# Performance work log

Hardware: AMD Instinct MI355X
Metric: run time of the kernel (lower is better)

Reference implementation:

```python
import jax, jax.numpy as jnp
import numpy as np

E = 1_600_000      # num edges
N = 50_000         # num nodes
G = 100            # num graphs in batch
EMB = 128          # emb_size
OUT = 256          # out_emb_size
NRAD = 6           # num_radial
NDENSE = 3         # num_dense


def setup_inputs() -> dict:
    key = jax.random.key(0)
    ks = jax.random.split(key, 8)
    m = jax.random.normal(ks[0], (E, EMB), dtype=jnp.float32)
    rbf = jax.random.normal(ks[1], (E, NRAD), dtype=jnp.float32)
    src = jax.random.randint(ks[2], (E,), 0, N, dtype=jnp.int64)
    graph_ids = jnp.sort(jax.random.randint(ks[3], (N,), 0, G, dtype=jnp.int64))
    # parameters (torch Linear convention: W [out, in])
    W_rbf = jax.random.normal(ks[4], (EMB, NRAD), dtype=jnp.float32) / np.sqrt(NRAD)
    W_up = jax.random.normal(ks[5], (OUT, EMB), dtype=jnp.float32) / np.sqrt(EMB)
    W_dense = jax.random.normal(ks[6], (NDENSE, OUT, OUT), dtype=jnp.float32) / np.sqrt(OUT)
    b_dense = jnp.zeros((NDENSE, OUT), dtype=jnp.float32)
    return {"m": m, "rbf": rbf, "src": src, "graph_ids": graph_ids,
            "W_rbf": W_rbf, "W_up": W_up, "W_dense": W_dense, "b_dense": b_dense}


def reference(m, rbf, src, graph_ids, W_rbf, W_up, W_dense, b_dense):
    # edge transform: tmp = m * dense_rbf(rbf)            [E, EMB]
    tmp = m * jnp.einsum('er,fr->ef', rbf, W_rbf)
    # reverse-graph copy_e/sum == scatter-sum onto original src nodes
    t = jax.ops.segment_sum(tmp, src, num_segments=N)     # [N, EMB]
    # up projection (no bias)
    t = jnp.einsum('ne,oe->no', t, W_up)                  # [N, OUT]
    # dense MLP with SiLU
    for i in range(NDENSE):
        t = jax.nn.silu(jnp.einsum('no,po->np', t, W_dense[i]) + b_dense[i])
    # extensive readout: per-graph sum
    out = jax.ops.segment_sum(t, graph_ids, num_segments=G)  # [G, OUT]
    return out
```

## Files before the change

### kernel.cpp

```cpp
#include <hip/hip_runtime.h>
#include <hip/hip_bf16.h>

typedef __attribute__((ext_vector_type(8))) short short8;
typedef __attribute__((ext_vector_type(4))) float f32x4;

#define EMB 128
#define OUT 256
#define NRAD 6
#define NDENSE 3
#define BSH 7
#define MAXBKT 512
#define HB 128

static __device__ __forceinline__ unsigned short f32_to_bf16(float f) {
    union { float f; unsigned u; } v; v.f = f;
    unsigned r = v.u + 0x7fffu + ((v.u >> 16) & 1u);
    return (unsigned short)(r >> 16);
}
static __device__ __forceinline__ float silu(float x) {
    return x / (1.f + __expf(-x));
}
static __device__ __forceinline__ void gload_lds16(const void* gp, void* lp) {
    __builtin_amdgcn_global_load_lds(
        (const __attribute__((address_space(1))) void*)gp,
        (__attribute__((address_space(3))) void*)lp, 16, 0, 0);
}

__global__ __launch_bounds__(256) void setup_hist_kernel(
        const int* __restrict__ src, int* __restrict__ bpart,
        const float* __restrict__ Wup, const float* __restrict__ Wd,
        unsigned short* __restrict__ Wbf, float* __restrict__ out,
        int E, int nbkt, int outn) {
    __shared__ int h[MAXBKT];
    for (int b = threadIdx.x; b < nbkt; b += 256) h[b] = 0;
    __syncthreads();
    int gtid = blockIdx.x * blockDim.x + threadIdx.x;
    int stride = gridDim.x * blockDim.x;
    for (int e = gtid; e < E; e += stride)
        atomicAdd(&h[src[e] >> BSH], 1);
    for (int j = gtid; j < outn; j += stride) out[j] = 0.f;
    const int n1 = OUT * EMB, n2 = NDENSE * OUT * OUT;
    for (int j = gtid; j < n1 + n2; j += stride)
        Wbf[j] = f32_to_bf16(j < n1 ? Wup[j] : Wd[j - n1]);
    __syncthreads();
    int* row = bpart + (size_t)blockIdx.x * MAXBKT;
    for (int b = threadIdx.x; b < nbkt; b += 256) row[b] = h[b];
}

__global__ __launch_bounds__(512) void bscan_kernel(
        const int* __restrict__ bpart, int* __restrict__ bbase,
        int* __restrict__ gcursor, int nbkt, int E) {
    __shared__ int s[MAXBKT];
    int t = threadIdx.x;
    int v = 0;
    if (t < nbkt) {
#pragma unroll 8
        for (int k = 0; k < HB; ++k) v += bpart[(size_t)k * MAXBKT + t];
    }
    s[t] = v;
    __syncthreads();
    for (int d = 1; d < MAXBKT; d <<= 1) {
        int x = (t >= d) ? s[t - d] : 0;
        __syncthreads();
        s[t] += x;
        __syncthreads();
    }
    if (t < nbkt) {
        int ex = s[t] - v;
        bbase[t] = ex;
        gcursor[t] = ex;
    }
    if (t == 0) bbase[nbkt] = E;
}

__global__ __launch_bounds__(256) void bscatter_kernel(
        const int* __restrict__ src, int* __restrict__ gcursor,
        int* __restrict__ pairs, int E, int nbkt) {
    __shared__ int h[MAXBKT];
    __shared__ int base[MAXBKT];
    for (int b = threadIdx.x; b < nbkt; b += 256) h[b] = 0;
    __syncthreads();
    const int per = (E + gridDim.x - 1) / gridDim.x;
    const int e0 = blockIdx.x * per;
    const int e1 = min(e0 + per, E);
    for (int e = e0 + threadIdx.x; e < e1; e += 256)
        atomicAdd(&h[src[e] >> BSH], 1);
    __syncthreads();
    for (int b = threadIdx.x; b < nbkt; b += 256)
        base[b] = h[b] ? atomicAdd(&gcursor[b], h[b]) : 0;
    __syncthreads();
    for (int e = e0 + threadIdx.x; e < e1; e += 256) {
        int s = src[e];
        int pos = atomicAdd(&base[s >> BSH], 1);
        pairs[pos] = (e << BSH) | (s & ((1 << BSH) - 1));
    }
}

__global__ __launch_bounds__(256) void local_csr_kernel(
        const int* __restrict__ pairs, const int* __restrict__ bbase,
        int* __restrict__ offsets, int* __restrict__ perm, int N, int E, int nbkt) {
    __shared__ int cnt[128], exc[128], cur[128];
    const int b = blockIdx.x;
    const int t = threadIdx.x;
    const int n0 = b << BSH;
    const int nn = min(128, N - n0);
    const int p0 = bbase[b], p1 = bbase[b + 1];
    if (t < 128) cnt[t] = 0;
    __syncthreads();
    for (int i = p0 + t; i < p1; i += 256)
        atomicAdd(&cnt[pairs[i] & 127], 1);
    __syncthreads();
    if (t < 128) exc[t] = cnt[t];
    __syncthreads();
    for (int d = 1; d < 128; d <<= 1) {
        int x = (t >= d && t < 128) ? exc[t - d] : 0;
        __syncthreads();
        if (t < 128) exc[t] += x;
        __syncthreads();
    }
    if (t < 128) {
        int ex = exc[t] - cnt[t];
        cur[t] = ex;
        if (t < nn) offsets[n0 + t] = p0 + ex;
    }
    if (b == 0 && t == 0) offsets[N] = E;
    __syncthreads();
    for (int i = p0 + t; i < p1; i += 256) {
        int pr = pairs[i];
        int pos = p0 + atomicAdd(&cur[pr & 127], 1);
        perm[pos] = pr >> BSH;
    }
}

__global__ __launch_bounds__(256) void edge_accum_kernel(
        const float* __restrict__ m, const float* __restrict__ rbf,
        const int* __restrict__ perm, const int* __restrict__ offsets,
        const float* __restrict__ W_rbf, uint2* __restrict__ t_pack, int N) {
    const int lane = threadIdx.x & 63;
    const int h = lane >> 5;
    const int c = lane & 31;
    const int gw = blockIdx.x * (blockDim.x >> 6) + (threadIdx.x >> 6);
    const int nwaves = gridDim.x * (blockDim.x >> 6);

    float wk[4][6];
#pragma unroll
    for (int k = 0; k < 4; ++k)
#pragma unroll
        for (int j = 0; j < 6; ++j) wk[k][j] = W_rbf[(4 * c + k) * NRAD + j];

    for (int node = gw; node < N; node += nwaves) {
        const int beg = offsets[node], end = offsets[node + 1];
        float a0 = 0.f, a1 = 0.f, a2 = 0.f, a3 = 0.f;
        int pe = 0;
        if (beg < end) {
            int pi = beg + (lane & 31); if (pi > end - 1) pi = end - 1;
            pe = perm[pi];
        }
        for (int cb = beg; cb < end; cb += 32) {
            int pe_next = 0;
            if (cb + 32 < end) {
                int pi = cb + 32 + (lane & 31); if (pi > end - 1) pi = end - 1;
                pe_next = perm[pi];
            }
            const int rem = end - cb;
            const int np = (rem >= 32) ? 16 : ((rem + 1) >> 1);
#pragma unroll 4
            for (int p = 0; p < np; ++p) {
                int e = __shfl(pe, 2 * p + h);
                const float2* rp = (const float2*)(rbf + (size_t)e * NRAD);
                float2 r0 = rp[0], r1 = rp[1], r2 = rp[2];
                float4 mv = *(const float4*)(m + (size_t)e * EMB + 4 * c);
                float g = (2 * p + h < rem) ? 1.f : 0.f;
                float p0 = (wk[0][0]*r0.x + wk[0][1]*r0.y + wk[0][2]*r1.x
                          + wk[0][3]*r1.y + wk[0][4]*r2.x + wk[0][5]*r2.y) * g;
                float p1 = (wk[1][0]*r0.x + wk[1][1]*r0.y + wk[1][2]*r1.x
                          + wk[1][3]*r1.y + wk[1][4]*r2.x + wk[1][5]*r2.y) * g;
                float p2 = (wk[2][0]*r0.x + wk[2][1]*r0.y + wk[2][2]*r1.x
                          + wk[2][3]*r1.y + wk[2][4]*r2.x + wk[2][5]*r2.y) * g;
                float p3 = (wk[3][0]*r0.x + wk[3][1]*r0.y + wk[3][2]*r1.x
                          + wk[3][3]*r1.y + wk[3][4]*r2.x + wk[3][5]*r2.y) * g;
                a0 = fmaf(mv.x, p0, a0);
                a1 = fmaf(mv.y, p1, a1);
                a2 = fmaf(mv.z, p2, a2);
                a3 = fmaf(mv.w, p3, a3);
            }
            pe = pe_next;
        }
        a0 += __shfl_xor(a0, 32);
        a1 += __shfl_xor(a1, 32);
        a2 += __shfl_xor(a2, 32);
        a3 += __shfl_xor(a3, 32);
        if (h == 0) {
            uint2 pk;
            pk.x = (unsigned)f32_to_bf16(a0) | ((unsigned)f32_to_bf16(a1) << 16);
            pk.y = (unsigned)f32_to_bf16(a2) | ((unsigned)f32_to_bf16(a3) << 16);
            t_pack[(size_t)node * 32 + c] = pk;
        }
    }
}

__global__ __launch_bounds__(512) void fused_mlp2_kernel(
        const unsigned short* __restrict__ A0,
        const unsigned short* __restrict__ Wup,
        const unsigned short* __restrict__ Wd,
        const float* __restrict__ bd,
        const int* __restrict__ gids,
        float* __restrict__ out, int M) {
    __shared__ char Abuf[65536];
    __shared__ char Wbuf[32768];
    const int t    = threadIdx.x;
    const int w    = t >> 6;
    const int lane = t & 63;
    const int r    = lane & 15;
    const int g    = lane >> 4;
    const int wrh  = (w >> 2) * 64;
    const int wc   = w & 3;
    const int row0 = blockIdx.x * 128;

    f32x4 acc[4][4];

#pragma unroll
    for (int it = 0; it < 4; ++it) {
        int unit = it * 512 + t;
        int row  = unit >> 4;
        int seg  = unit & 15;
        int csrc = (seg * 16) ^ ((row & 7) << 4);
        int ga = row0 + row; if (ga >= M) ga = M - 1;
        gload_lds16((const char*)A0 + (size_t)ga * 256 + csrc, Abuf + unit * 16);
    }

#pragma unroll
    for (int i = 0; i < 4; ++i)
#pragma unroll
        for (int j = 0; j < 4; ++j) acc[i][j] = (f32x4){0.f, 0.f, 0.f, 0.f};
#pragma unroll
    for (int kci = 0; kci < 2; ++kci) {
        const int kc = kci * 64;
        if (kci) __syncthreads();
#pragma unroll
        for (int it = 0; it < 4; ++it) {
            int unit = it * 512 + t;
            int wrow = unit >> 3;
            int seg  = unit & 7;
            int csrc = (seg * 16) ^ ((wrow & 7) << 4);
            gload_lds16((const char*)Wup + (size_t)wrow * 256 + kc * 2 + csrc,
                        Wbuf + unit * 16);
        }
        asm volatile("s_waitcnt vmcnt(0)" ::: "memory");
        __syncthreads();
#pragma unroll
        for (int ks = 0; ks < 2; ++ks) {
            short8 af[4], bf[4];
#pragma unroll
            for (int mi = 0; mi < 4; ++mi) {
                int row = wrh + mi * 16 + r;
                int off = kc * 2 + ks * 64 + g * 16;
                af[mi] = *(const short8*)(Abuf + row * 256 + (off ^ ((row & 7) << 4)));
            }
#pragma unroll
            for (int nj = 0; nj < 4; ++nj) {
                int col = wc * 64 + nj * 16 + r;
                bf[nj] = *(const short8*)(Wbuf + col * 128
                          + ((ks * 64 + g * 16) ^ ((col & 7) << 4)));
            }
#pragma unroll
            for (int mi = 0; mi < 4; ++mi)
#pragma unroll
                for (int nj = 0; nj < 4; ++nj)
                    acc[mi][nj] = __builtin_amdgcn_mfma_f32_16x16x32_bf16(
                        af[mi], bf[nj], acc[mi][nj], 0, 0, 0);
        }
    }
    __syncthreads();
#pragma unroll
    for (int mi = 0; mi < 4; ++mi)
#pragma unroll
        for (int nj = 0; nj < 4; ++nj)
#pragma unroll
            for (int q = 0; q < 4; ++q) {
                int row = wrh + mi * 16 + g * 4 + q;
                int col = wc * 64 + nj * 16 + r;
                *(unsigned short*)(Abuf + row * 512 + ((col * 2) ^ ((row & 7) << 4)))
                    = f32_to_bf16(acc[mi][nj][q]);
            }
    __syncthreads();

    for (int ell = 0; ell < NDENSE; ++ell) {
        const unsigned short* Wl = Wd + (size_t)ell * OUT * OUT;
        const float* bias = bd + ell * OUT;
#pragma unroll
        for (int i = 0; i < 4; ++i)
#pragma unroll
            for (int j = 0; j < 4; ++j) acc[i][j] = (f32x4){0.f, 0.f, 0.f, 0.f};
#pragma unroll
        for (int kci = 0; kci < 4; ++kci) {
            const int kc = kci * 64;
            __syncthreads();
#pragma unroll
            for (int it = 0; it < 4; ++it) {
                int unit = it * 512 + t;
                int wrow = unit >> 3;
                int seg  = unit & 7;
                int csrc = (seg * 16) ^ ((wrow & 7) << 4);
                gload_lds16((const char*)Wl + (size_t)wrow * 512 + kc * 2 + csrc,
                            Wbuf + unit * 16);
            }
            asm volatile("s_waitcnt vmcnt(0)" ::: "memory");
            __syncthreads();
#pragma unroll
            for (int ks = 0; ks < 2; ++ks) {
                short8 af[4], bf[4];
#pragma unroll
                for (int mi = 0; mi < 4; ++mi) {
                    int row = wrh + mi * 16 + r;
                    int off = kc * 2 + ks * 64 + g * 16;
                    af[mi] = *(const short8*)(Abuf + row * 512 + (off ^ ((row & 7) << 4)));
                }
#pragma unroll
                for (int nj = 0; nj < 4; ++nj) {
                    int col = wc * 64 + nj * 16 + r;
                    bf[nj] = *(const short8*)(Wbuf + col * 128
                              + ((ks * 64 + g * 16) ^ ((col & 7) << 4)));
                }
#pragma unroll
                for (int mi = 0; mi < 4; ++mi)
#pragma unroll
                    for (int nj = 0; nj < 4; ++nj)
                        acc[mi][nj] = __builtin_amdgcn_mfma_f32_16x16x32_bf16(
                            af[mi], bf[nj], acc[mi][nj], 0, 0, 0);
            }
        }
        __syncthreads();
        if (ell < NDENSE - 1) {
#pragma unroll
            for (int mi = 0; mi < 4; ++mi)
#pragma unroll
                for (int nj = 0; nj < 4; ++nj) {
                    int col = wc * 64 + nj * 16 + r;
                    float b = bias[col];
#pragma unroll
                    for (int q = 0; q < 4; ++q) {
                        int row = wrh + mi * 16 + g * 4 + q;
                        *(unsigned short*)(Abuf + row * 512
                            + ((col * 2) ^ ((row & 7) << 4)))
                            = f32_to_bf16(silu(acc[mi][nj][q] + b));
                    }
                }
            __syncthreads();
        } else {
            bool uni = (row0 + 127 < M) && (gids[row0] == gids[row0 + 127]);
            if (uni) {
                int gph = gids[row0];
                float* og = out + (size_t)gph * OUT;
#pragma unroll
                for (int nj = 0; nj < 4; ++nj) {
                    int gcol = wc * 64 + nj * 16 + r;
                    float b = bias[gcol];
                    float s = 0.f;
#pragma unroll
                    for (int mi = 0; mi < 4; ++mi)
#pragma unroll
                        for (int q = 0; q < 4; ++q)
                            s += silu(acc[mi][nj][q] + b);
                    s += __shfl_xor(s, 16);
                    s += __shfl_xor(s, 32);
                    if (g == 0) atomicAdd(&og[gcol], s);
                }
            } else {
#pragma unroll
                for (int nj = 0; nj < 4; ++nj) {
                    int gcol = wc * 64 + nj * 16 + r;
                    float b = bias[gcol];
#pragma unroll
                    for (int mi = 0; mi < 4; ++mi)
#pragma unroll
                        for (int q = 0; q < 4; ++q) {
                            int grow = row0 + wrh + mi * 16 + g * 4 + q;
                            if (grow < M)
                                atomicAdd(&out[(size_t)gids[grow] * OUT + gcol],
                                          silu(acc[mi][nj][q] + b));
                        }
                }
            }
        }
    }
}

extern "C" void kernel_launch(void* const* d_in, const int* in_sizes, int n_in,
                              void* d_out, int out_size, void* d_ws, size_t ws_size,
                              hipStream_t stream) {
    const float* m         = (const float*)d_in[0];
    const float* rbf       = (const float*)d_in[1];
    const int*   src       = (const int*)d_in[2];
    const int*   gids      = (const int*)d_in[3];
    const float* W_rbf     = (const float*)d_in[4];
    const float* W_up      = (const float*)d_in[5];
    const float* W_dense   = (const float*)d_in[6];
    const float* b_dense   = (const float*)d_in[7];
    float* out = (float*)d_out;

    const int E = in_sizes[2];
    const int N = in_sizes[3];
    const int nbkt = (N + 127) >> BSH;

    size_t off = 0;
    auto alloc = [&](size_t bytes) -> void* {
        void* p = (char*)d_ws + off;
        off += (bytes + 255) & ~(size_t)255;
        return p;
    };
    int* bpart   = (int*)alloc((size_t)HB * MAXBKT * 4);
    int* bbase   = (int*)alloc((size_t)(MAXBKT + 1) * 4);
    int* gcursor = (int*)alloc((size_t)MAXBKT * 4);
    int* offsets = (int*)alloc(((size_t)N + 1) * 4);
    int* pairs   = (int*)alloc((size_t)E * 4);
    int* perm    = (int*)alloc((size_t)E * 4);
    unsigned short* t_bf = (unsigned short*)alloc((size_t)N * EMB * 2);
    unsigned short* Wbf  = (unsigned short*)alloc((size_t)(OUT * EMB + NDENSE * OUT * OUT) * 2);
    unsigned short* Wup_bf = Wbf;
    unsigned short* Wd_bf  = Wbf + OUT * EMB;

    setup_hist_kernel<<<HB, 256, 0, stream>>>(src, bpart, W_up, W_dense, Wbf,
                                              out, E, nbkt, out_size);
    bscan_kernel<<<1, MAXBKT, 0, stream>>>(bpart, bbase, gcursor, nbkt, E);
    bscatter_kernel<<<512, 256, 0, stream>>>(src, gcursor, pairs, E, nbkt);
    local_csr_kernel<<<nbkt, 256, 0, stream>>>(pairs, bbase, offsets, perm, N, E, nbkt);

    edge_accum_kernel<<<2048, 256, 0, stream>>>(m, rbf, perm, offsets, W_rbf,
                                                (uint2*)t_bf, N);

    fused_mlp2_kernel<<<(N + 127) / 128, 512, 0, stream>>>(t_bf, Wup_bf, Wd_bf,
                                                           b_dense, gids, out, N);
}
```

Baseline: 397.7 us.

## Reuse per-block histograms in scatter and double-buffer MLP weight staging

The bucket scatter no longer recomputes a per-block histogram and global cursor atomics. The scan turns each histogram block's counts into exclusive per-block offsets, and the scatter uses the same grid-stride partition to place edges directly; the histogram grid also grows to more blocks. The fused MLP kernel double-buffers weight tiles in LDS, prefetching the next k-chunk (and the next layer's first chunk) while MFMAs run on the current one. This drops a barrier per chunk at the cost of doubling the weight LDS buffer, which may reduce occupancy.

```diff
diff --git a/kernel.cpp b/kernel.cpp
--- a/kernel.cpp
+++ b/kernel.cpp
@@ -10,7 +10,7 @@
 #define NDENSE 3
 #define BSH 7
 #define MAXBKT 512
-#define HB 128
+#define HB 256
 
 static __device__ __forceinline__ unsigned short f32_to_bf16(float f) {
     union { float f; unsigned u; } v; v.f = f;
@@ -24,6 +24,17 @@
     __builtin_amdgcn_global_load_lds(
         (const __attribute__((address_space(1))) void*)gp,
         (__attribute__((address_space(3))) void*)lp, 16, 0, 0);
+}
+static __device__ __forceinline__ void stage_w(const char* Wsrc, int rowBytes,
+                                               int kcByte, char* dst, int t) {
+#pragma unroll
+    for (int it = 0; it < 4; ++it) {
+        int unit = it * 512 + t;
+        int wrow = unit >> 3;
+        int seg  = unit & 7;
+        int csrc = (seg * 16) ^ ((wrow & 7) << 4);
+        gload_lds16(Wsrc + (size_t)wrow * rowBytes + kcByte + csrc, dst + unit * 16);
+    }
 }
 
 __global__ __launch_bounds__(256) void setup_hist_kernel(
@@ -48,14 +59,16 @@
 }
 
 __global__ __launch_bounds__(512) void bscan_kernel(
-        const int* __restrict__ bpart, int* __restrict__ bbase,
-        int* __restrict__ gcursor, int nbkt, int E) {
+        int* __restrict__ bpart, int* __restrict__ bbase, int nbkt, int E) {
     __shared__ int s[MAXBKT];
     int t = threadIdx.x;
     int v = 0;
     if (t < nbkt) {
-#pragma unroll 8
-        for (int k = 0; k < HB; ++k) v += bpart[(size_t)k * MAXBKT + t];
+        for (int k = 0; k < HB; ++k) {
+            int x = bpart[(size_t)k * MAXBKT + t];
+            bpart[(size_t)k * MAXBKT + t] = v;
+            v += x;
+        }
     }
     s[t] = v;
     __syncthreads();
@@ -65,31 +78,21 @@
         s[t] += x;
         __syncthreads();
     }
-    if (t < nbkt) {
-        int ex = s[t] - v;
-        bbase[t] = ex;
-        gcursor[t] = ex;
-    }
+    if (t < nbkt) bbase[t] = s[t] - v;
     if (t == 0) bbase[nbkt] = E;
 }
 
 __global__ __launch_bounds__(256) void bscatter_kernel(
-        const int* __restrict__ src, int* __restrict__ gcursor,
-        int* __restrict__ pairs, int E, int nbkt) {
-    __shared__ int h[MAXBKT];
+        const int* __restrict__ src, const int* __restrict__ bpart,
+        const int* __restrict__ bbase, int* __restrict__ pairs, int E, int nbkt) {
     __shared__ int base[MAXBKT];
-    for (int b = threadIdx.x; b < nbkt; b += 256) h[b] = 0;
-    __syncthreads();
-    const int per = (E + gridDim.x - 1) / gridDim.x;
-    const int e0 = blockIdx.x * per;
-    const int e1 = min(e0 + per, E);
-    for (int e = e0 + threadIdx.x; e < e1; e += 256)
-        atomicAdd(&h[src[e] >> BSH], 1);
-    __syncthreads();
-    for (int b = threadIdx.x; b < nbkt; b += 256)
-        base[b] = h[b] ? atomicAdd(&gcursor[b], h[b]) : 0;
-    __syncthreads();
-    for (int e = e0 + threadIdx.x; e < e1; e += 256) {
+    const int b = blockIdx.x;
+    const int* myrow = bpart + (size_t)b * MAXBKT;
+    for (int bb = threadIdx.x; bb < nbkt; bb += 256)
+        base[bb] = myrow[bb] + bbase[bb];
+    __syncthreads();
+    int gtid = b * 256 + threadIdx.x, gs = HB * 256;
+    for (int e = gtid; e < E; e += gs) {
         int s = src[e];
         int pos = atomicAdd(&base[s >> BSH], 1);
         pairs[pos] = (e << BSH) | (s & ((1 << BSH) - 1));
@@ -207,7 +210,7 @@
         const int* __restrict__ gids,
         float* __restrict__ out, int M) {
     __shared__ char Abuf[65536];
-    __shared__ char Wbuf[32768];
+    __shared__ char Wbuf[2][32768];
     const int t    = threadIdx.x;
     const int w    = t >> 6;
     const int lane = t & 63;
@@ -229,6 +232,9 @@
         gload_lds16((const char*)A0 + (size_t)ga * 256 + csrc, Abuf + unit * 16);
     }
 
+    int p = 0;
+    stage_w((const char*)Wup, 256, 0, Wbuf[0], t);
+
 #pragma unroll
     for (int i = 0; i < 4; ++i)
 #pragma unroll
@@ -236,18 +242,10 @@
 #pragma unroll
     for (int kci = 0; kci < 2; ++kci) {
         const int kc = kci * 64;
-        if (kci) __syncthreads();
-#pragma unroll
-        for (int it = 0; it < 4; ++it) {
-            int unit = it * 512 + t;
-            int wrow = unit >> 3;
-            int seg  = unit & 7;
-            int csrc = (seg * 16) ^ ((wrow & 7) << 4);
-            gload_lds16((const char*)Wup + (size_t)wrow * 256 + kc * 2 + csrc,
-                        Wbuf + unit * 16);
-        }
         asm volatile("s_waitcnt vmcnt(0)" ::: "memory");
         __syncthreads();
+        if (kci + 1 < 2)
+            stage_w((const char*)Wup, 256, (kci + 1) * 128, Wbuf[p ^ 1], t);
 #pragma unroll
         for (int ks = 0; ks < 2; ++ks) {
             short8 af[4], bf[4];
@@ -260,7 +258,7 @@
 #pragma unroll
             for (int nj = 0; nj < 4; ++nj) {
                 int col = wc * 64 + nj * 16 + r;
-                bf[nj] = *(const short8*)(Wbuf + col * 128
+                bf[nj] = *(const short8*)(Wbuf[p] + col * 128
                           + ((ks * 64 + g * 16) ^ ((col & 7) << 4)));
             }
 #pragma unroll
@@ -270,7 +268,9 @@
                     acc[mi][nj] = __builtin_amdgcn_mfma_f32_16x16x32_bf16(
                         af[mi], bf[nj], acc[mi][nj], 0, 0, 0);
         }
-    }
+        p ^= 1;
+    }
+    stage_w((const char*)Wd, 512, 0, Wbuf[p], t);
     __syncthreads();
 #pragma unroll
     for (int mi = 0; mi < 4; ++mi)
@@ -286,7 +286,7 @@
     __syncthreads();
 
     for (int ell = 0; ell < NDENSE; ++ell) {
-        const unsigned short* Wl = Wd + (size_t)ell * OUT * OUT;
+        const char* Wl = (const char*)(Wd + (size_t)ell * OUT * OUT);
         const float* bias = bd + ell * OUT;
 #pragma unroll
         for (int i = 0; i < 4; ++i)
@@ -295,18 +295,10 @@
 #pragma unroll
         for (int kci = 0; kci < 4; ++kci) {
             const int kc = kci * 64;
-            __syncthreads();
-#pragma unroll
-            for (int it = 0; it < 4; ++it) {
-                int unit = it * 512 + t;
-                int wrow = unit >> 3;
-                int seg  = unit & 7;
-                int csrc = (seg * 16) ^ ((wrow & 7) << 4);
-                gload_lds16((const char*)Wl + (size_t)wrow * 512 + kc * 2 + csrc,
-                            Wbuf + unit * 16);
-            }
             asm volatile("s_waitcnt vmcnt(0)" ::: "memory");
             __syncthreads();
+            if (kci + 1 < 4)
+                stage_w(Wl, 512, (kci + 1) * 128, Wbuf[p ^ 1], t);
 #pragma unroll
             for (int ks = 0; ks < 2; ++ks) {
                 short8 af[4], bf[4];
@@ -319,7 +311,7 @@
 #pragma unroll
                 for (int nj = 0; nj < 4; ++nj) {
                     int col = wc * 64 + nj * 16 + r;
-                    bf[nj] = *(const short8*)(Wbuf + col * 128
+                    bf[nj] = *(const short8*)(Wbuf[p] + col * 128
                               + ((ks * 64 + g * 16) ^ ((col & 7) << 4)));
                 }
 #pragma unroll
@@ -329,9 +321,12 @@
                         acc[mi][nj] = __builtin_amdgcn_mfma_f32_16x16x32_bf16(
                             af[mi], bf[nj], acc[mi][nj], 0, 0, 0);
             }
-        }
-        __syncthreads();
+            p ^= 1;
+        }
         if (ell < NDENSE - 1) {
+            stage_w((const char*)(Wd + (size_t)(ell + 1) * OUT * OUT), 512, 0,
+                    Wbuf[p], t);
+            __syncthreads();
 #pragma unroll
             for (int mi = 0; mi < 4; ++mi)
 #pragma unroll
@@ -411,7 +406,6 @@
     };
     int* bpart   = (int*)alloc((size_t)HB * MAXBKT * 4);
     int* bbase   = (int*)alloc((size_t)(MAXBKT + 1) * 4);
-    int* gcursor = (int*)alloc((size_t)MAXBKT * 4);
     int* offsets = (int*)alloc(((size_t)N + 1) * 4);
     int* pairs   = (int*)alloc((size_t)E * 4);
     int* perm    = (int*)alloc((size_t)E * 4);
@@ -422,8 +416,8 @@
 
     setup_hist_kernel<<<HB, 256, 0, stream>>>(src, bpart, W_up, W_dense, Wbf,
                                               out, E, nbkt, out_size);
-    bscan_kernel<<<1, MAXBKT, 0, stream>>>(bpart, bbase, gcursor, nbkt, E);
-    bscatter_kernel<<<512, 256, 0, stream>>>(src, gcursor, pairs, E, nbkt);
+    bscan_kernel<<<1, MAXBKT, 0, stream>>>(bpart, bbase, nbkt, E);
+    bscatter_kernel<<<HB, 256, 0, stream>>>(src, bpart, bbase, pairs, E, nbkt);
     local_csr_kernel<<<nbkt, 256, 0, stream>>>(pairs, bbase, offsets, perm, N, E, nbkt);
 
     edge_accum_kernel<<<2048, 256, 0, stream>>>(m, rbf, perm, offsets, W_rbf,
```

After: 384.7 us (median of 2 runs). 3.3% less time.
